# Performance work log

Measured on AMD Instinct MI355X. Metric: run time of the kernel, lower is better.

## Reference

```python
import jax, jax.numpy as jnp
import numpy as np

BITS = 4
GROUP = 128
K = 8192      # infeatures
N = 28672     # outfeatures
M = 32        # batch of tokens (decode-style small M)


def setup_inputs() -> dict:
    key = jax.random.key(0)
    k1, k2, k3, k4 = jax.random.split(key, 4)
    A = jax.random.normal(k1, (M, K), dtype=jnp.float16)
    # packed uint4 weights: two nibbles per byte, stored as int32 holding 0..255
    qweight = jax.random.randint(k2, (N, K // 2), 0, 256, dtype=jnp.int32)
    scales = (jax.random.normal(k3, (N, K // GROUP)) * 0.01).astype(jnp.float16)
    zeros = (jax.random.uniform(k4, (N, K // GROUP)) * 15.0).astype(jnp.float16)
    bias = jnp.zeros((N,), dtype=jnp.float16)
    return {"A": A, "qweight": qweight, "scales": scales, "zeros": zeros, "bias": bias}


def _dequantize(qweight, scales, zeros):
    # unpack two uint4 values per byte, low nibble first (matches unpack_qzeros order)
    low = qweight & 15
    high = (qweight >> 4) & 15
    w_int = jnp.stack([low, high], axis=-1).reshape(qweight.shape[0], -1)  # (N, K)
    w = w_int.astype(jnp.float16)
    n, k = w.shape
    wg = w.reshape(n, k // GROUP, GROUP)
    # 'original' zeros type: (w - zero) * scale, per (out_channel, group)
    wd = (wg - zeros[:, :, None]) * scales[:, :, None]
    return wd.reshape(n, k)  # (N, K) fp16


def reference(A, qweight, scales, zeros, bias):
    W = _dequantize(qweight, scales, zeros)          # (N, K)
    C = jnp.einsum("mk,nk->mn", A, W) + bias[None, :]  # (M, N)
    return C.astype(A.dtype)
```

## Files before the change

### kernel.cpp

```cpp
#include <hip/hip_runtime.h>

#define KK 8192
#define NN 28672
#define MM 32
#define GRP 128
#define NBLK 32
#define NBLOCKS (NN / NBLK)
#define TILEK 128
#define WTILES 16

typedef __bf16 bf16;
typedef bf16  bf16x8 __attribute__((ext_vector_type(8)));
typedef float floatx4 __attribute__((ext_vector_type(4)));

__global__ __launch_bounds__(256, 4) void qgemm_kernel(
    const float* __restrict__ A, const int* __restrict__ qw,
    const float* __restrict__ scales, const float* __restrict__ zeros,
    const float* __restrict__ bias, float* __restrict__ out) {
  __shared__ float red[3][64][16];

  const int tid = threadIdx.x;
  const int wv  = tid >> 6;
  const int l   = tid & 63;
  const int lr  = l & 15;
  const int lg  = l >> 4;
  const int n0  = blockIdx.x * NBLK;

  const int kb_e = wv * 2048;
  const int kb_i = wv * 1024;

  floatx4 acc[2][2];
#pragma unroll
  for (int a = 0; a < 2; ++a)
#pragma unroll
    for (int b = 0; b < 2; ++b) acc[a][b] = (floatx4){0.f, 0.f, 0.f, 0.f};

  for (int t = 0; t < WTILES; ++t) {
    const int g = wv * WTILES + t;

    const float s0 = scales[(n0 + lr) * 64 + g];
    const float z0 = zeros [(n0 + lr) * 64 + g];
    const float s1 = scales[(n0 + 16 + lr) * 64 + g];
    const float z1 = zeros [(n0 + 16 + lr) * 64 + g];
    const float c1[2] = {s0, s1};
    const float c0[2] = {-(128.f + z0) * s0, -(128.f + z1) * s1};

    bf16x8 af[2][4];
#pragma unroll
    for (int s = 0; s < 4; ++s) {
#pragma unroll
      for (int mt = 0; mt < 2; ++mt) {
        const float* ap = A + (mt * 16 + lr) * KK + kb_e + t * TILEK + s * 32 + lg * 8;
        const float4 fa = *(const float4*)(ap);
        const float4 fb = *(const float4*)(ap + 4);
        bf16x8 f;
        f[0] = (bf16)fa.x; f[1] = (bf16)fa.y; f[2] = (bf16)fa.z; f[3] = (bf16)fa.w;
        f[4] = (bf16)fb.x; f[5] = (bf16)fb.y; f[6] = (bf16)fb.z; f[7] = (bf16)fb.w;
        af[mt][s] = f;
      }
    }

#pragma unroll
    for (int s = 0; s < 4; ++s) {
#pragma unroll
      for (int nt = 0; nt < 2; ++nt) {
        const uint4 v = *(const uint4*)(qw + (n0 + nt * 16 + lr) * 4096 + kb_i + t * 64 + (s * 4 + lg) * 4);
        bf16x8 bfr;
#pragma unroll
        for (int i = 0; i < 4; ++i) {
          const unsigned q = ((const unsigned*)&v)[i];
          const float lo = __builtin_bit_cast(float, 0x43000000u | ((q & 0x0Fu) << 16));
          const float hi = __builtin_bit_cast(float, 0x43000000u | ((q & 0xF0u) << 12));
          bfr[2 * i]     = (bf16)__builtin_fmaf(lo, c1[nt], c0[nt]);
          bfr[2 * i + 1] = (bf16)__builtin_fmaf(hi, c1[nt], c0[nt]);
        }
#pragma unroll
        for (int mt = 0; mt < 2; ++mt)
          acc[mt][nt] = __builtin_amdgcn_mfma_f32_16x16x32_bf16(af[mt][s], bfr, acc[mt][nt], 0, 0, 0);
      }
    }
  }

  if (wv > 0) {
#pragma unroll
    for (int mt = 0; mt < 2; ++mt)
#pragma unroll
      for (int nt = 0; nt < 2; ++nt)
#pragma unroll
        for (int r = 0; r < 4; ++r)
          red[wv - 1][l][mt * 8 + nt * 4 + r] = acc[mt][nt][r];
  }
  __syncthreads();
  if (wv == 0) {
#pragma unroll
    for (int mt = 0; mt < 2; ++mt)
#pragma unroll
      for (int nt = 0; nt < 2; ++nt)
#pragma unroll
        for (int r = 0; r < 4; ++r) {
          float v = acc[mt][nt][r];
#pragma unroll
          for (int w2 = 0; w2 < 3; ++w2) v += red[w2][l][mt * 8 + nt * 4 + r];
          const int m = mt * 16 + lg * 4 + r;
          const int n = n0 + nt * 16 + lr;
          out[m * NN + n] = v + bias[n];
        }
  }
}

extern "C" void kernel_launch(void* const* d_in, const int* in_sizes, int n_in,
                              void* d_out, int out_size, void* d_ws, size_t ws_size,
                              hipStream_t stream) {
  const float* A    = (const float*)d_in[0];
  const int*   qw   = (const int*)d_in[1];
  const float* sc   = (const float*)d_in[2];
  const float* zr   = (const float*)d_in[3];
  const float* bias = (const float*)d_in[4];
  float*       out  = (float*)d_out;

  qgemm_kernel<<<dim3(NBLOCKS), dim3(256), 0, stream>>>(A, qw, sc, zr, bias, out);
}
```

Baseline: 738.0 us.

## Pre-convert activations to bf16 and halve N per block

Adds a separate kernel that converts A from fp32 to bf16 into the workspace once, so the GEMM kernel loads bf16 fragments directly instead of converting fp32 in every block. The N tile per block shrinks from 32 to 16, doubling the grid. Scales and zeros are now loaded as float4 vectors covering four groups at once. A-fragment loads move into the inner loop, and the extra launch plus the smaller tile reduce A reuse per block in exchange for more parallelism and fewer registers.

```diff
diff --git a/kernel.cpp b/kernel.cpp
--- a/kernel.cpp
+++ b/kernel.cpp
@@ -3,21 +3,30 @@
 #define KK 8192
 #define NN 28672
 #define MM 32
-#define GRP 128
-#define NBLK 32
+#define NBLK 16
 #define NBLOCKS (NN / NBLK)
-#define TILEK 128
 #define WTILES 16
 
 typedef __bf16 bf16;
 typedef bf16  bf16x8 __attribute__((ext_vector_type(8)));
 typedef float floatx4 __attribute__((ext_vector_type(4)));
 
+__global__ __launch_bounds__(256) void aconv_kernel(const float* __restrict__ A,
+                                                    bf16* __restrict__ Ab) {
+  const int i = (blockIdx.x * 256 + threadIdx.x) * 8;
+  const float4 fa = *(const float4*)(A + i);
+  const float4 fb = *(const float4*)(A + i + 4);
+  bf16x8 o;
+  o[0] = (bf16)fa.x; o[1] = (bf16)fa.y; o[2] = (bf16)fa.z; o[3] = (bf16)fa.w;
+  o[4] = (bf16)fb.x; o[5] = (bf16)fb.y; o[6] = (bf16)fb.z; o[7] = (bf16)fb.w;
+  *(bf16x8*)(Ab + i) = o;
+}
+
 __global__ __launch_bounds__(256, 4) void qgemm_kernel(
-    const float* __restrict__ A, const int* __restrict__ qw,
+    const bf16* __restrict__ Ab, const int* __restrict__ qw,
     const float* __restrict__ scales, const float* __restrict__ zeros,
     const float* __restrict__ bias, float* __restrict__ out) {
-  __shared__ float red[3][64][16];
+  __shared__ float red[3][64][8];
 
   const int tid = threadIdx.x;
   const int wv  = tid >> 6;
@@ -28,55 +37,43 @@
 
   const int kb_e = wv * 2048;
   const int kb_i = wv * 1024;
+  const int gb   = wv * WTILES;
 
-  floatx4 acc[2][2];
-#pragma unroll
-  for (int a = 0; a < 2; ++a)
-#pragma unroll
-    for (int b = 0; b < 2; ++b) acc[a][b] = (floatx4){0.f, 0.f, 0.f, 0.f};
+  const float4* sp = (const float4*)(scales + (n0 + lr) * 64 + gb);
+  const float4* zp = (const float4*)(zeros  + (n0 + lr) * 64 + gb);
 
-  for (int t = 0; t < WTILES; ++t) {
-    const int g = wv * WTILES + t;
-
-    const float s0 = scales[(n0 + lr) * 64 + g];
-    const float z0 = zeros [(n0 + lr) * 64 + g];
-    const float s1 = scales[(n0 + 16 + lr) * 64 + g];
-    const float z1 = zeros [(n0 + 16 + lr) * 64 + g];
-    const float c1[2] = {s0, s1};
-    const float c0[2] = {-(128.f + z0) * s0, -(128.f + z1) * s1};
-
-    bf16x8 af[2][4];
-#pragma unroll
-    for (int s = 0; s < 4; ++s) {
-#pragma unroll
-      for (int mt = 0; mt < 2; ++mt) {
-        const float* ap = A + (mt * 16 + lr) * KK + kb_e + t * TILEK + s * 32 + lg * 8;
-        const float4 fa = *(const float4*)(ap);
-        const float4 fb = *(const float4*)(ap + 4);
-        bf16x8 f;
-        f[0] = (bf16)fa.x; f[1] = (bf16)fa.y; f[2] = (bf16)fa.z; f[3] = (bf16)fa.w;
-        f[4] = (bf16)fb.x; f[5] = (bf16)fb.y; f[6] = (bf16)fb.z; f[7] = (bf16)fb.w;
-        af[mt][s] = f;
-      }
-    }
+  floatx4 acc[2];
+  acc[0] = (floatx4){0.f, 0.f, 0.f, 0.f};
+  acc[1] = (floatx4){0.f, 0.f, 0.f, 0.f};
 
 #pragma unroll
-    for (int s = 0; s < 4; ++s) {
+  for (int q = 0; q < 4; ++q) {
+    const float4 sv = sp[q];
+    const float4 zv = zp[q];
 #pragma unroll
-      for (int nt = 0; nt < 2; ++nt) {
-        const uint4 v = *(const uint4*)(qw + (n0 + nt * 16 + lr) * 4096 + kb_i + t * 64 + (s * 4 + lg) * 4);
+    for (int u = 0; u < 4; ++u) {
+      const int t = q * 4 + u;
+      const float c1 = (u == 0) ? sv.x : (u == 1) ? sv.y : (u == 2) ? sv.z : sv.w;
+      const float zz = (u == 0) ? zv.x : (u == 1) ? zv.y : (u == 2) ? zv.z : zv.w;
+      const float c0 = -(128.f + zz) * c1;
+
+#pragma unroll
+      for (int s = 0; s < 4; ++s) {
+        const uint4 v = *(const uint4*)(qw + (n0 + lr) * 4096 + kb_i + t * 64 + (s * 4 + lg) * 4);
         bf16x8 bfr;
 #pragma unroll
         for (int i = 0; i < 4; ++i) {
-          const unsigned q = ((const unsigned*)&v)[i];
-          const float lo = __builtin_bit_cast(float, 0x43000000u | ((q & 0x0Fu) << 16));
-          const float hi = __builtin_bit_cast(float, 0x43000000u | ((q & 0xF0u) << 12));
-          bfr[2 * i]     = (bf16)__builtin_fmaf(lo, c1[nt], c0[nt]);
-          bfr[2 * i + 1] = (bf16)__builtin_fmaf(hi, c1[nt], c0[nt]);
+          const unsigned qd = ((const unsigned*)&v)[i];
+          const float lo = __builtin_bit_cast(float, 0x43000000u | ((qd & 0x0Fu) << 16));
+          const float hi = __builtin_bit_cast(float, 0x43000000u | ((qd & 0xF0u) << 12));
+          bfr[2 * i]     = (bf16)__builtin_fmaf(lo, c1, c0);
+          bfr[2 * i + 1] = (bf16)__builtin_fmaf(hi, c1, c0);
         }
 #pragma unroll
-        for (int mt = 0; mt < 2; ++mt)
-          acc[mt][nt] = __builtin_amdgcn_mfma_f32_16x16x32_bf16(af[mt][s], bfr, acc[mt][nt], 0, 0, 0);
+        for (int mt = 0; mt < 2; ++mt) {
+          const bf16x8 af = *(const bf16x8*)(Ab + (mt * 16 + lr) * KK + kb_e + t * 128 + s * 32 + lg * 8);
+          acc[mt] = __builtin_amdgcn_mfma_f32_16x16x32_bf16(af, bfr, acc[mt], 0, 0, 0);
+        }
       }
     }
   }
@@ -85,26 +82,22 @@
 #pragma unroll
     for (int mt = 0; mt < 2; ++mt)
 #pragma unroll
-      for (int nt = 0; nt < 2; ++nt)
-#pragma unroll
-        for (int r = 0; r < 4; ++r)
-          red[wv - 1][l][mt * 8 + nt * 4 + r] = acc[mt][nt][r];
+      for (int r = 0; r < 4; ++r)
+        red[wv - 1][l][mt * 4 + r] = acc[mt][r];
   }
   __syncthreads();
   if (wv == 0) {
 #pragma unroll
     for (int mt = 0; mt < 2; ++mt)
 #pragma unroll
-      for (int nt = 0; nt < 2; ++nt)
+      for (int r = 0; r < 4; ++r) {
+        float v = acc[mt][r];
 #pragma unroll
-        for (int r = 0; r < 4; ++r) {
-          float v = acc[mt][nt][r];
-#pragma unroll
-          for (int w2 = 0; w2 < 3; ++w2) v += red[w2][l][mt * 8 + nt * 4 + r];
-          const int m = mt * 16 + lg * 4 + r;
-          const int n = n0 + nt * 16 + lr;
-          out[m * NN + n] = v + bias[n];
-        }
+        for (int w2 = 0; w2 < 3; ++w2) v += red[w2][l][mt * 4 + r];
+        const int m = mt * 16 + lg * 4 + r;
+        const int n = n0 + lr;
+        out[m * NN + n] = v + bias[n];
+      }
   }
 }
 
@@ -117,6 +110,8 @@
   const float* zr   = (const float*)d_in[3];
   const float* bias = (const float*)d_in[4];
   float*       out  = (float*)d_out;
+  bf16*        Ab   = (bf16*)d_ws;
 
-  qgemm_kernel<<<dim3(NBLOCKS), dim3(256), 0, stream>>>(A, qw, sc, zr, bias, out);
+  aconv_kernel<<<dim3(MM * KK / (256 * 8)), dim3(256), 0, stream>>>(A, Ab);
+  qgemm_kernel<<<dim3(NBLOCKS), dim3(256), 0, stream>>>(Ab, qw, sc, zr, bias, out);
 }
```

After: 698.5 us. 1.06x faster.
